# Performance work log

Hardware: AMD Instinct MI355X
Metric: run time of the kernel (lower is better)

## Reference

```python
import jax, jax.numpy as jnp
import numpy as np

FEAT_STRIDE = 16
PRE_NMS = 6000
POST_NMS = 300
NMS_THRESH = 0.7


def _whctrs(a):
    w = a[2] - a[0] + 1.0
    h = a[3] - a[1] + 1.0
    return w, h, a[0] + 0.5 * (w - 1), a[1] + 0.5 * (h - 1)

def _mkanchors(ws, hs, xc, yc):
    return np.stack([xc - 0.5 * (ws - 1), yc - 0.5 * (hs - 1),
                     xc + 0.5 * (ws - 1), yc + 0.5 * (hs - 1)], axis=1)

def _ratio_enum(anchor, ratios):
    w, h, xc, yc = _whctrs(anchor)
    size = w * h
    ws = np.round(np.sqrt(size / ratios))
    hs = np.round(ws * ratios)
    return _mkanchors(ws, hs, xc, yc)

def _scale_enum(anchor, scales):
    w, h, xc, yc = _whctrs(anchor)
    return _mkanchors(w * scales, h * scales, xc, yc)

def generate_anchors(base_size=16, ratios=np.array([0.5, 1.0, 2.0]), scales=np.array([8, 16, 32])):
    base = np.array([1, 1, base_size, base_size], dtype=np.float64) - 1
    ra = _ratio_enum(base, np.asarray(ratios, np.float64))
    return np.vstack([_scale_enum(ra[i], np.asarray(scales, np.float64)) for i in range(ra.shape[0])])


def setup_inputs() -> dict:
    key = jax.random.key(0)
    k1, k2 = jax.random.split(key)
    B, A, H, W = 8, 9, 64, 64
    scores = jax.random.normal(k1, (B, 2 * A, H, W), jnp.float32)
    bbox_deltas = jax.random.normal(k2, (B, 4 * A, H, W), jnp.float32)
    anchors = jnp.asarray(generate_anchors(16), jnp.float32)  # [9, 4]
    return {"scores": scores, "bbox_deltas": bbox_deltas, "anchors": anchors,
            "image_width": 1024, "image_height": 1024}


def _nms_keep(iou, thresh):
    # greedy NMS on score-sorted boxes given a full IoU matrix
    n = iou.shape[0]
    idx = jnp.arange(n)
    def body(i, keep):
        sup = keep[i] & (iou[i] > thresh) & (idx > i)
        return keep & ~sup
    return jax.lax.fori_loop(0, n, body, jnp.ones((n,), bool))


def _nms_one(boxes):  # boxes [PRE_NMS, 4], sorted by score desc
    b = jax.lax.stop_gradient(boxes)
    area = (b[:, 2] - b[:, 0] + 1.0) * (b[:, 3] - b[:, 1] + 1.0)
    iw = jnp.clip(jnp.minimum(b[:, None, 2], b[None, :, 2]) -
                  jnp.maximum(b[:, None, 0], b[None, :, 0]) + 1.0, 0.0)
    ih = jnp.clip(jnp.minimum(b[:, None, 3], b[None, :, 3]) -
                  jnp.maximum(b[:, None, 1], b[None, :, 1]) + 1.0, 0.0)
    inter = iw * ih
    iou = inter / (area[:, None] + area[None, :] - inter)
    keep = _nms_keep(iou, NMS_THRESH)
    # compact kept boxes to the front, pad with zeros (fixed shape)
    rank = jnp.cumsum(keep) - 1
    dest = jnp.where(keep, rank, PRE_NMS)  # suppressed -> dump row
    out = jnp.zeros((PRE_NMS + 1, 4), boxes.dtype).at[dest].set(boxes)
    return out[:POST_NMS]


def _forward(scores, bbox_deltas, anchors, image_width, image_height):
    B = scores.shape[0]
    A = anchors.shape[0]
    H, W = scores.shape[2], scores.shape[3]
    fg = scores[:, A:, :, :]                                   # [B, A, H, W]
    # shifted anchor grid
    mx, my = jnp.meshgrid(jnp.arange(W) * FEAT_STRIDE, jnp.arange(H) * FEAT_STRIDE)
    shifts = jnp.stack([mx.ravel(), my.ravel(), mx.ravel(), my.ravel()], 1).astype(scores.dtype)
    all_anchors = (shifts[:, None, :] + anchors[None, :, :]).reshape(-1, 4)  # [K*A, 4]
    deltas = bbox_deltas.transpose(0, 2, 3, 1).reshape(B, -1, 4)             # [B, K*A, 4]
    sc = fg.transpose(0, 2, 3, 1).reshape(B, -1)                             # [B, K*A]
    # bbox_transform_inv
    aw = all_anchors[:, 2] - all_anchors[:, 0] + 1.0
    ah = all_anchors[:, 3] - all_anchors[:, 1] + 1.0
    acx = all_anchors[:, 0] + 0.5 * aw
    acy = all_anchors[:, 1] + 0.5 * ah
    pcx = deltas[..., 0] * aw + acx
    pcy = deltas[..., 1] * ah + acy
    pw = jnp.exp(deltas[..., 2]) * aw
    ph = jnp.exp(deltas[..., 3]) * ah
    # clip to image
    x1 = jnp.clip(pcx - 0.5 * pw, 0.0, image_width - 1)
    y1 = jnp.clip(pcy - 0.5 * ph, 0.0, image_height - 1)
    x2 = jnp.clip(pcx + 0.5 * pw, 0.0, image_width - 1)
    y2 = jnp.clip(pcy + 0.5 * ph, 0.0, image_height - 1)
    proposals = jnp.stack([x1, y1, x2, y2], -1)                 # [B, K*A, 4]
    # per-image pre-NMS top-k by score
    _, order = jax.lax.top_k(sc, PRE_NMS)
    boxes = jnp.take_along_axis(proposals, order[..., None], axis=1)  # [B, PRE, 4]
    props = jax.lax.map(_nms_one, boxes)                        # [B, POST, 4]
    bidx = jnp.broadcast_to(jnp.arange(B, dtype=props.dtype)[:, None, None], (B, POST_NMS, 1))
    return jnp.concatenate([bidx, props], axis=-1)              # [B, POST, 5]


def reference(scores, bbox_deltas, anchors, image_width, image_height):
    return _forward(scores, bbox_deltas, anchors, image_width, image_height)
```

## Files before the change

### kernel.cpp

```cpp
#include <hip/hip_runtime.h>
#include <math.h>

#pragma clang fp contract(off)

#define BB 8
#define AA 9
#define NPIX 4096
#define NN (NPIX*AA)
#define PRE 6000
#define POST 300
#define SELCAP 7000
#define HWORDS 16384
#define TMAX 10111

#define RA 0x3F000000u
#define RB 0x41000000u
__device__ __forceinline__ unsigned key_bin(unsigned k) {
    unsigned bin;
    if (k < RA)      bin = k >> 17;
    else if (k < RB) bin = 8064u + ((k - RA) >> 14);
    else             bin = 10112u + ((k - RB) >> 17);
    return (bin > 32767u) ? 32767u : bin;
}

#define SMEM_BYTES 65536

__device__ __forceinline__ unsigned score_key(float s) {
    unsigned fb = __float_as_uint(s);
    unsigned u = (fb & 0x80000000u) ? ~fb : (fb | 0x80000000u);
    return ~u;
}

__device__ __forceinline__ unsigned phalf(unsigned v, unsigned bin) {
    return (v >> ((bin & 1) << 4)) & 0xFFFFu;
}

__device__ __forceinline__ bool iou_gt(float ax1, float ay1, float ax2, float ay2, float aa,
                                       float bx1_, float by1_, float bx2_, float by2_, float ab) {
    float xx1 = fmaxf(ax1, bx1_);
    float yy1 = fmaxf(ay1, by1_);
    float xx2 = fminf(ax2, bx2_);
    float yy2 = fminf(ay2, by2_);
    float iw = fmaxf(xx2 - xx1 + 1.0f, 0.0f);
    float ih = fmaxf(yy2 - yy1 + 1.0f, 0.0f);
    float inter = iw * ih;
    float uni = (aa + ab) - inter;
    return (double)inter >= 0x1.666667p-1 * (double)uni;
}

__device__ __forceinline__ void decode_box(int g, const unsigned short* sorted16,
                                           const float* anch, const float* deltas_b,
                                           float fw, float fh, float4* bx, float* ar) {
    unsigned idx = sorted16[(g < PRE) ? g : (PRE - 1)];
    int a = (int)(idx % AA);
    int pix = (int)(idx / AA);
    int wq = pix & 63, hq = pix >> 6;
    float sx = (float)(wq * 16), sy = (float)(hq * 16);
    float ax1 = anch[a * 4 + 0] + sx, ay1 = anch[a * 4 + 1] + sy;
    float ax2 = anch[a * 4 + 2] + sx, ay2 = anch[a * 4 + 3] + sy;
    float aw = ax2 - ax1 + 1.0f, ah = ay2 - ay1 + 1.0f;
    float acx = ax1 + 0.5f * aw, acy = ay1 + 0.5f * ah;
    const float* dp = deltas_b + (size_t)(a * 4) * NPIX + pix;
    float d0 = dp[0], d1 = dp[NPIX], d2 = dp[2 * NPIX], d3 = dp[3 * NPIX];
    float pcx = d0 * aw + acx, pcy = d1 * ah + acy;
    float pw = expf(d2) * aw, ph = expf(d3) * ah;
    float x1 = fminf(fmaxf(pcx - 0.5f * pw, 0.0f), fw);
    float y1 = fminf(fmaxf(pcy - 0.5f * ph, 0.0f), fh);
    float x2 = fminf(fmaxf(pcx + 0.5f * pw, 0.0f), fw);
    float y2 = fminf(fmaxf(pcy + 0.5f * ph, 0.0f), fh);
    *bx = make_float4(x1, y1, x2, y2);
    *ar = (x2 - x1 + 1.0f) * (y2 - y1 + 1.0f);
}

__global__ __launch_bounds__(1024) void proposal_kernel(const float* __restrict__ scores,
                                                        const float* __restrict__ deltas,
                                                        const float* __restrict__ anchors,
                                                        const int* __restrict__ imw,
                                                        const int* __restrict__ imh,
                                                        float* __restrict__ out) {
    __shared__ __align__(16) unsigned char smem[SMEM_BYTES];
    unsigned*       hist32 = (unsigned*)smem;
    unsigned*       keyh   = (unsigned*)(smem + 20480);
    unsigned short* idxl   = (unsigned short*)(smem + 48512);
    unsigned*       scal   = (unsigned*)(smem + 65344);
    unsigned short* sorted16 = (unsigned short*)(smem + 20480);
    float4*         kb4  = (float4*)smem;
    float*          kba  = (float*)(smem + 4800);
    float4*         cnd4 = (float4*)(smem + 6016);
    float*          cnda = (float*)(smem + 8064);
    unsigned long long* srow  = (unsigned long long*)(smem + 8576);
    unsigned long long* deadw = (unsigned long long*)(smem + 9088);
    float*          anch = (float*)(smem + 9216);

    int b = blockIdx.x;
    int tid = threadIdx.x;
    int wave = tid >> 6, lane = tid & 63;
    const float* sc = scores + (size_t)(b * (2 * AA) + AA) * NPIX;
    const float4* sc4 = (const float4*)sc;
    const float* deltas_b = deltas + (size_t)b * (4 * AA) * NPIX;
    float fw = (float)(imw[0] - 1);
    float fh = (float)(imh[0] - 1);

    unsigned kc[36];
    for (int j = tid; j < HWORDS; j += 1024) hist32[j] = 0;
    __syncthreads();
    #pragma unroll
    for (int q = 0; q < 9; ++q) {
        float4 v = sc4[(q << 10) + tid];
        kc[q * 4 + 0] = score_key(v.x);
        kc[q * 4 + 1] = score_key(v.y);
        kc[q * 4 + 2] = score_key(v.z);
        kc[q * 4 + 3] = score_key(v.w);
        #pragma unroll
        for (int c = 0; c < 4; ++c) {
            unsigned bin = key_bin(kc[q * 4 + c]);
            atomicAdd(&hist32[bin >> 1], 1u << ((bin & 1) << 4));
        }
    }
    __syncthreads();

    const unsigned* hw = hist32 + tid * 16;
    unsigned ssum = 0;
    #pragma unroll
    for (int j = 0; j < 16; ++j) { unsigned w = hw[j]; ssum += (w & 0xFFFFu) + (w >> 16); }
    __syncthreads();
    unsigned x = ssum;
    #pragma unroll
    for (int d = 1; d < 64; d <<= 1) {
        unsigned y = __shfl_up(x, (unsigned)d, 64);
        if (lane >= d) x += y;
    }
    if (lane == 63) scal[wave] = x;
    __syncthreads();
    unsigned wexcl = 0;
    #pragma unroll
    for (int w = 0; w < 16; ++w) if (w < wave) wexcl += scal[w];
    unsigned gexcl = wexcl + (x - ssum);
    unsigned gincl = gexcl + ssum;
    if (gexcl <= (PRE - 1) && (PRE - 1) < gincl) {
        unsigned c = gexcl, T = tid * 32, tot = gincl;
        bool f = false;
        for (int j = 0; j < 32 && !f; ++j) {
            unsigned d = phalf(hw[j >> 1], (unsigned)j);
            if ((PRE - 1) < c + d) { T = tid * 32 + j; tot = c + d; f = true; }
            c += d;
        }
        scal[16] = T;
        scal[17] = tot;
    }
    __syncthreads();
    unsigned T = scal[16];
    if (T > TMAX) T = TMAX;
    unsigned cnt = scal[17];
    if (cnt > SELCAP) cnt = SELCAP;

    if ((unsigned)(tid * 32) <= T) {
        unsigned run = gexcl;
        unsigned* wv = hist32 + tid * 16;
        #pragma unroll
        for (int j = 0; j < 16; ++j) {
            unsigned v = wv[j];
            unsigned c0 = v & 0xFFFFu, c1 = v >> 16;
            wv[j] = run | ((run + c0) << 16);
            run += c0 + c1;
        }
    }
    __syncthreads();

    #pragma unroll
    for (int q2 = 0; q2 < 36; ++q2) {
        unsigned k = kc[q2];
        unsigned bin = key_bin(k);
        if (bin <= T) {
            unsigned old = atomicAdd(&hist32[bin >> 1], 1u << ((bin & 1) << 4));
            unsigned pos = phalf(old, bin);
            if (pos < SELCAP) {
                keyh[pos] = k;
                int a = q2 >> 2;
                int pix = (tid << 2) + (q2 & 3);
                idxl[pos] = (unsigned short)(pix * AA + a);
            }
        }
    }
    __syncthreads();

    unsigned rnk8[8], id8[8];
    #pragma unroll
    for (int m = 0; m < 8; ++m) {
        int s = (m << 10) + tid;
        rnk8[m] = 0xFFFFFFFFu;
        if (s < (int)cnt) {
            unsigned k = keyh[s];
            unsigned id = idxl[s];
            unsigned bin = key_bin(k);
            unsigned start = bin ? phalf(hist32[(bin - 1) >> 1], bin - 1) : 0u;
            unsigned end = phalf(hist32[bin >> 1], bin);
            if (end > cnt) end = cnt;
            if (start > end) start = end;
            unsigned rank = start;
            for (unsigned j = start; j < end; ++j) {
                unsigned kj = keyh[j];
                rank += (kj < k) ? 1u : 0u;
                if (kj == k) rank += ((unsigned)idxl[j] < id) ? 1u : 0u;
            }
            rnk8[m] = rank;
            id8[m] = id;
        }
    }
    __syncthreads();
    #pragma unroll
    for (int m = 0; m < 8; ++m)
        if (rnk8[m] < PRE) sorted16[rnk8[m]] = (unsigned short)id8[m];
    if (tid < 36) anch[tid] = anchors[tid];
    __syncthreads();

    if (tid < 64) {
        float4 bx; float ar;
        decode_box(tid, sorted16, anch, deltas_b, fw, fh, &bx, &ar);
        cnd4[tid] = bx; cnda[tid] = ar;
    }
    __syncthreads();

    int cur = 0, K = 0, p = 0;
    for (;;) {
        float4 mc = cnd4[p * 64 + lane];
        float ma = cnda[p * 64 + lane];

        float4 nb; float na;
        if (wave == 8)
            decode_box(cur + 64 + lane, sorted16, anch, deltas_b, fw, fh, &nb, &na);

        bool dead = (cur + lane >= PRE);
        for (int k = wave; k < K; k += 16) {
            float4 kv = kb4[k];
            float ka = kba[k];
            dead = dead || iou_gt(kv.x, kv.y, kv.z, kv.w, ka, mc.x, mc.y, mc.z, mc.w, ma);
        }
        unsigned long long db = __ballot(dead);
        if (lane == 0) deadw[wave] = db;
        if (wave == 8) {
            cnd4[(p ^ 1) * 64 + lane] = nb;
            cnda[(p ^ 1) * 64 + lane] = na;
        }
        __syncthreads();

        unsigned long long dk = deadw[0];
        #pragma unroll
        for (int w = 1; w < 16; ++w) dk |= deadw[w];

        if (dk != ~0ULL) {
            #pragma unroll
            for (int q2 = 0; q2 < 4; ++q2) {
                int j = (q2 << 4) + wave;
                if (!((dk >> j) & 1ULL)) {
                    float4 cj = cnd4[p * 64 + j];
                    float aj = cnda[p * 64 + j];
                    bool g = (lane < j) && iou_gt(mc.x, mc.y, mc.z, mc.w, ma,
                                                  cj.x, cj.y, cj.z, cj.w, aj);
                    unsigned long long bl = __ballot(g);
                    if (lane == 0) srow[j] = bl;
                }
            }
            __syncthreads();

            unsigned long long row = srow[lane];
            unsigned long long live = ~dk;
            unsigned long long keptb = 0ULL;
            int allowed = POST - K;
            while (live) {
                int f = __ffsll((long long)live) - 1;
                keptb |= (1ULL << f);
                if (__popcll(keptb) >= allowed) break;
                bool die = (row >> f) & 1ULL;
                unsigned long long dbl = __ballot(die);
                live &= ~(dbl | (1ULL << f));
            }
            int nkeep = __popcll(keptb);
            int take = (nkeep < allowed) ? nkeep : allowed;

            if (wave == 0 && ((keptb >> lane) & 1ULL)) {
                int rnk = __popcll(keptb & ((1ULL << lane) - 1ULL));
                if (rnk < take) { kb4[K + rnk] = mc; kba[K + rnk] = ma; }
            }
            K += take;
        }

        cur += 64;
        p ^= 1;
        if (K >= POST || cur >= PRE) break;
        __syncthreads();
    }

    __syncthreads();
    for (int idx = tid; idx < POST * 5; idx += 1024) {
        int row_ = idx / 5;
        int col = idx - row_ * 5;
        float val = 0.0f;
        if (row_ < K) {
            float4 v = kb4[row_];
            val = (col == 0) ? (float)b : (col == 1) ? v.x : (col == 2) ? v.y
                : (col == 3) ? v.z : v.w;
        }
        out[(size_t)b * POST * 5 + idx] = val;
    }
}

extern "C" void kernel_launch(void* const* d_in, const int* in_sizes, int n_in,
                              void* d_out, int out_size, void* d_ws, size_t ws_size,
                              hipStream_t stream) {
    const float* scores  = (const float*)d_in[0];
    const float* deltas  = (const float*)d_in[1];
    const float* anchors = (const float*)d_in[2];
    const int*   imw     = (const int*)d_in[3];
    const int*   imh     = (const int*)d_in[4];
    float* out = (float*)d_out;

    proposal_kernel<<<BB, 1024, 0, stream>>>(scores, deltas, anchors, imw, imh, out);
}
```

Baseline: 154.7 us.

## Compute intra-chunk suppression matrix before barrier and drop per-score register cache

The 64x64 intra-chunk IoU suppression rows are now computed unconditionally before the first barrier, alongside the kept-box test, which removes the second __syncthreads per NMS iteration. The 36 cached score keys are no longer held in registers; scores are re-read from global memory and re-keyed in the scatter pass to cut register pressure. In exchange, every chunk pays the full intra-chunk IoU work even when all candidates are already dead, and the scores are loaded from global memory twice.

```diff
diff --git a/kernel.cpp b/kernel.cpp
--- a/kernel.cpp
+++ b/kernel.cpp
@@ -101,21 +101,19 @@
     float fw = (float)(imw[0] - 1);
     float fh = (float)(imh[0] - 1);
 
-    unsigned kc[36];
     for (int j = tid; j < HWORDS; j += 1024) hist32[j] = 0;
     __syncthreads();
     #pragma unroll
     for (int q = 0; q < 9; ++q) {
         float4 v = sc4[(q << 10) + tid];
-        kc[q * 4 + 0] = score_key(v.x);
-        kc[q * 4 + 1] = score_key(v.y);
-        kc[q * 4 + 2] = score_key(v.z);
-        kc[q * 4 + 3] = score_key(v.w);
-        #pragma unroll
-        for (int c = 0; c < 4; ++c) {
-            unsigned bin = key_bin(kc[q * 4 + c]);
-            atomicAdd(&hist32[bin >> 1], 1u << ((bin & 1) << 4));
-        }
+        unsigned b0 = key_bin(score_key(v.x));
+        unsigned b1 = key_bin(score_key(v.y));
+        unsigned b2 = key_bin(score_key(v.z));
+        unsigned b3 = key_bin(score_key(v.w));
+        atomicAdd(&hist32[b0 >> 1], 1u << ((b0 & 1) << 4));
+        atomicAdd(&hist32[b1 >> 1], 1u << ((b1 & 1) << 4));
+        atomicAdd(&hist32[b2 >> 1], 1u << ((b2 & 1) << 4));
+        atomicAdd(&hist32[b3 >> 1], 1u << ((b3 & 1) << 4));
     }
     __syncthreads();
 
@@ -168,17 +166,21 @@
     __syncthreads();
 
     #pragma unroll
-    for (int q2 = 0; q2 < 36; ++q2) {
-        unsigned k = kc[q2];
-        unsigned bin = key_bin(k);
-        if (bin <= T) {
-            unsigned old = atomicAdd(&hist32[bin >> 1], 1u << ((bin & 1) << 4));
-            unsigned pos = phalf(old, bin);
-            if (pos < SELCAP) {
-                keyh[pos] = k;
-                int a = q2 >> 2;
-                int pix = (tid << 2) + (q2 & 3);
-                idxl[pos] = (unsigned short)(pix * AA + a);
+    for (int q = 0; q < 9; ++q) {
+        float4 v = sc4[(q << 10) + tid];
+        #pragma unroll
+        for (int c = 0; c < 4; ++c) {
+            float s = (c == 0) ? v.x : (c == 1) ? v.y : (c == 2) ? v.z : v.w;
+            unsigned k = score_key(s);
+            unsigned bin = key_bin(k);
+            if (bin <= T) {
+                unsigned old = atomicAdd(&hist32[bin >> 1], 1u << ((bin & 1) << 4));
+                unsigned pos = phalf(old, bin);
+                if (pos < SELCAP) {
+                    keyh[pos] = k;
+                    int pix = (tid << 2) + c;
+                    idxl[pos] = (unsigned short)(pix * AA + q);
+                }
             }
         }
     }
@@ -238,6 +240,17 @@
         }
         unsigned long long db = __ballot(dead);
         if (lane == 0) deadw[wave] = db;
+
+        #pragma unroll
+        for (int q2 = 0; q2 < 4; ++q2) {
+            int j = (q2 << 4) + wave;
+            float4 cj = cnd4[p * 64 + j];
+            float aj = cnda[p * 64 + j];
+            bool g = (lane < j) && iou_gt(mc.x, mc.y, mc.z, mc.w, ma,
+                                          cj.x, cj.y, cj.z, cj.w, aj);
+            unsigned long long bl = __ballot(g);
+            if (lane == 0) srow[j] = bl;
+        }
         if (wave == 8) {
             cnd4[(p ^ 1) * 64 + lane] = nb;
             cnda[(p ^ 1) * 64 + lane] = na;
@@ -247,47 +260,29 @@
         unsigned long long dk = deadw[0];
         #pragma unroll
         for (int w = 1; w < 16; ++w) dk |= deadw[w];
-
-        if (dk != ~0ULL) {
-            #pragma unroll
-            for (int q2 = 0; q2 < 4; ++q2) {
-                int j = (q2 << 4) + wave;
-                if (!((dk >> j) & 1ULL)) {
-                    float4 cj = cnd4[p * 64 + j];
-                    float aj = cnda[p * 64 + j];
-                    bool g = (lane < j) && iou_gt(mc.x, mc.y, mc.z, mc.w, ma,
-                                                  cj.x, cj.y, cj.z, cj.w, aj);
-                    unsigned long long bl = __ballot(g);
-                    if (lane == 0) srow[j] = bl;
-                }
-            }
-            __syncthreads();
-
-            unsigned long long row = srow[lane];
-            unsigned long long live = ~dk;
-            unsigned long long keptb = 0ULL;
-            int allowed = POST - K;
-            while (live) {
-                int f = __ffsll((long long)live) - 1;
-                keptb |= (1ULL << f);
-                if (__popcll(keptb) >= allowed) break;
-                bool die = (row >> f) & 1ULL;
-                unsigned long long dbl = __ballot(die);
-                live &= ~(dbl | (1ULL << f));
-            }
-            int nkeep = __popcll(keptb);
-            int take = (nkeep < allowed) ? nkeep : allowed;
-
-            if (wave == 0 && ((keptb >> lane) & 1ULL)) {
-                int rnk = __popcll(keptb & ((1ULL << lane) - 1ULL));
-                if (rnk < take) { kb4[K + rnk] = mc; kba[K + rnk] = ma; }
-            }
-            K += take;
-        }
-
+        unsigned long long row = srow[lane];
+        unsigned long long live = ~dk;
+        unsigned long long keptb = 0ULL;
+        int allowed = POST - K;
+        while (live) {
+            int f = __ffsll((long long)live) - 1;
+            keptb |= (1ULL << f);
+            if (__popcll(keptb) >= allowed) break;
+            bool die = (row >> f) & 1ULL;
+            unsigned long long dbl = __ballot(die);
+            live &= ~(dbl | (1ULL << f));
+        }
+        int nkeep = __popcll(keptb);
+        int take = (nkeep < allowed) ? nkeep : allowed;
+
+        if (wave == 0 && ((keptb >> lane) & 1ULL)) {
+            int rnk = __popcll(keptb & ((1ULL << lane) - 1ULL));
+            if (rnk < take) { kb4[K + rnk] = mc; kba[K + rnk] = ma; }
+        }
+        K += take;
         cur += 64;
+        if (K >= POST || cur >= PRE) break;
         p ^= 1;
-        if (K >= POST || cur >= PRE) break;
         __syncthreads();
     }
 
```

New measurement: 150.8 us. -2.5%, faster.
